# Optimization experiments

Hardware: AMD Instinct MI355X
Metric: run time of the kernel (lower is better)

The kernel has to match this reference:

```python
import jax, jax.numpy as jnp
import numpy as np

B, C, D = 65536, 64, 32

def setup_inputs() -> dict:
    key = jax.random.key(0)
    k1, k2 = jax.random.split(key)
    x = jax.random.normal(k1, (B, C, D), dtype=jnp.float32)
    W = jax.random.normal(k2, (C, D, D), dtype=jnp.float32)  # stacked per-channel Linear weights (torch inits to eye, but trainable)
    return {"x": x, "W": W}

def reference(x, W):
    # x: [B, C, D]; W: [C, D, D] with W[j] the weight of the j-th Linear(D,D,bias=False)
    Dd = W.shape[-1]
    b = x.shape[0]
    xr = x.reshape(b, -1, Dd)           # [B, C, D]
    xT = jnp.swapaxes(xr, 1, 2)          # [B, D, C] (k=D axis, channel last)
    # Ox[b,k,j] = sum_m W[j,k,m] * xT[b,m,j]  (per-channel tiny GEMM, batched)
    Ox = jnp.einsum('jkm,bmj->bkj', W, xT)
    # xOx[b,i] = sum_k sum_j xT[b,k,i] * Ox[b,k,j]
    xOx = jnp.einsum('bki,bkj->bi', xT, Ox)  # [B, C]
    return jnp.tanh(xOx)
```

## Files before the change

kernel.cpp:

```cpp
#include <hip/hip_runtime.h>
#include <cstdint>

typedef __attribute__((ext_vector_type(8))) short short8;
typedef __attribute__((ext_vector_type(4))) float f32x4;

__device__ __forceinline__ unsigned short bf16_rne(float f) {
    unsigned u = __float_as_uint(f);
    u += 0x7FFFu + ((u >> 16) & 1u);
    return (unsigned short)(u >> 16);
}

__global__ __launch_bounds__(1024) void wtab_kernel(const float* __restrict__ W,
                                                    unsigned short* __restrict__ tab) {
    int el = blockIdx.x * 1024 + threadIdx.x;
    int b    = el & 7;
    int lane = (el >> 3) & 63;
    int nh   = (el >> 9) & 1;
    int ks   = el >> 10;
    int e = ks * 32 + (lane >> 4) * 8 + b;
    int k = nh * 16 + (lane & 15);
    int jp = e >> 5, m = e & 31;
    float w = W[jp * 1024 + k * 32 + m];
    unsigned short hi = bf16_rne(w);
    float fh = __uint_as_float((unsigned)hi << 16);
    unsigned short lo = bf16_rne(w - fh);
    tab[(((ks * 2 + nh) * 2 + 0) * 64 + lane) * 8 + b] = hi;
    tab[(((ks * 2 + nh) * 2 + 1) * 64 + lane) * 8 + b] = lo;
}

__device__ __forceinline__ void split8(const float4& a, const float4& b,
                                       short8& hi, short8& lo) {
    float f[8] = {a.x, a.y, a.z, a.w, b.x, b.y, b.z, b.w};
    #pragma unroll
    for (int u = 0; u < 8; ++u) {
        unsigned short h = bf16_rne(f[u]);
        hi[u] = (short)h;
        float fh = __uint_as_float((unsigned)h << 16);
        lo[u] = (short)bf16_rne(f[u] - fh);
    }
}

__global__ __launch_bounds__(256) void ipf_kernel(const float* __restrict__ x,
                                                  const unsigned short* __restrict__ tab,
                                                  float* __restrict__ out) {
    __shared__ float Sl[4][16 * 36];
    const int t = threadIdx.x;
    const int w = t >> 6, l = t & 63;
    const long long b0 = ((long long)blockIdx.x * 4 + w) * 16;

    const float* xrow = x + (b0 + (l & 15)) * 2048 + (l >> 4) * 8;
    f32x4 c0 = {0.f, 0.f, 0.f, 0.f};
    f32x4 c1 = {0.f, 0.f, 0.f, 0.f};

    #pragma unroll 2
    for (int ks = 0; ks < 64; ++ks) {
        const float4 xa = *(const float4*)(xrow + ks * 32);
        const float4 xb = *(const float4*)(xrow + ks * 32 + 4);
        const short8* tp = (const short8*)(tab + ks * 2048);
        const short8 wh0 = tp[l];
        const short8 wl0 = tp[64 + l];
        const short8 wh1 = tp[128 + l];
        const short8 wl1 = tp[192 + l];
        short8 xhi, xlo;
        split8(xa, xb, xhi, xlo);
        c0 = __builtin_amdgcn_mfma_f32_16x16x32_bf16(xhi, wh0, c0, 0, 0, 0);
        c1 = __builtin_amdgcn_mfma_f32_16x16x32_bf16(xhi, wh1, c1, 0, 0, 0);
        c0 = __builtin_amdgcn_mfma_f32_16x16x32_bf16(xhi, wl0, c0, 0, 0, 0);
        c1 = __builtin_amdgcn_mfma_f32_16x16x32_bf16(xhi, wl1, c1, 0, 0, 0);
        c0 = __builtin_amdgcn_mfma_f32_16x16x32_bf16(xlo, wh0, c0, 0, 0, 0);
        c1 = __builtin_amdgcn_mfma_f32_16x16x32_bf16(xlo, wh1, c1, 0, 0, 0);
    }

    float* S = &Sl[w][0];
    #pragma unroll
    for (int r = 0; r < 4; ++r) {
        S[((l >> 4) * 4 + r) * 36 + (l & 15)]      = c0[r];
        S[((l >> 4) * 4 + r) * 36 + 16 + (l & 15)] = c1[r];
    }
    asm volatile("s_waitcnt lgkmcnt(0)" ::: "memory");

    const float* xb2 = x + b0 * 2048;
    #pragma unroll 1
    for (int r = 0; r < 16; ++r) {
        const float* xr = xb2 + r * 2048 + l * 32;
        const float* sr = S + r * 36;
        float s = 0.0f;
        #pragma unroll
        for (int q = 0; q < 8; ++q) {
            const float4 xv = *(const float4*)(xr + q * 4);
            s += xv.x * sr[q * 4] + xv.y * sr[q * 4 + 1]
               + xv.z * sr[q * 4 + 2] + xv.w * sr[q * 4 + 3];
        }
        const float e2 = __expf(2.0f * s);
        out[(b0 + r) * 64 + l] = 1.0f - 2.0f / (e2 + 1.0f);
    }
}

extern "C" void kernel_launch(void* const* d_in, const int* in_sizes, int n_in,
                              void* d_out, int out_size, void* d_ws, size_t ws_size,
                              hipStream_t stream) {
    const float* x = (const float*)d_in[0];
    const float* W = (const float*)d_in[1];
    float* out = (float*)d_out;
    unsigned short* tab = (unsigned short*)d_ws;

    wtab_kernel<<<64, 1024, 0, stream>>>(W, tab);
    ipf_kernel<<<1024, 256, 0, stream>>>(x, tab, out);
}
```

Before: 207.2 us.

## Stream x through LDS ring buffer with async global-to-LDS loads, reuse for second phase

Restructures the main kernel to process 256 batch rows per block, streaming x into an 18-slot LDS ring buffer via global_load_lds with swizzled addresses and a two-deep prefetch. The first-phase MFMA work is split across waves by k-half and ks-half, with partial sums folded through LDS. The second dot product then reads x back from LDS instead of global memory, lagging 16 slots behind. This removes the second global read of x and overlaps loads with compute, at the cost of many barriers per iteration, one block per CU, and a large LDS footprint.

```diff
diff --git a/kernel.cpp b/kernel.cpp
--- a/kernel.cpp
+++ b/kernel.cpp
@@ -3,6 +3,12 @@
 
 typedef __attribute__((ext_vector_type(8))) short short8;
 typedef __attribute__((ext_vector_type(4))) float f32x4;
+typedef const __attribute__((address_space(1))) uint32_t gu32;
+typedef __attribute__((address_space(3))) uint32_t lu32;
+
+#define NB    18
+#define CHB   8192
+#define NSLOT 256
 
 __device__ __forceinline__ unsigned short bf16_rne(float f) {
     unsigned u = __float_as_uint(f);
@@ -28,6 +34,12 @@
     tab[(((ks * 2 + nh) * 2 + 1) * 64 + lane) * 8 + b] = lo;
 }
 
+template <int CTRL>
+__device__ __forceinline__ float dpp_add(float v) {
+    int moved = __builtin_amdgcn_update_dpp(0, __float_as_int(v), CTRL, 0xF, 0xF, true);
+    return v + __int_as_float(moved);
+}
+
 __device__ __forceinline__ void split8(const float4& a, const float4& b,
                                        short8& hi, short8& lo) {
     float f[8] = {a.x, a.y, a.z, a.w, b.x, b.y, b.z, b.w};
@@ -40,60 +52,121 @@
     }
 }
 
-__global__ __launch_bounds__(256) void ipf_kernel(const float* __restrict__ x,
-                                                  const unsigned short* __restrict__ tab,
-                                                  float* __restrict__ out) {
-    __shared__ float Sl[4][16 * 36];
+__global__ __launch_bounds__(256, 1) void ipf_kernel(const float* __restrict__ x,
+                                                     const unsigned short* __restrict__ tab,
+                                                     float* __restrict__ out) {
+    extern __shared__ char smem[];
+    char* xbuf = smem;
+    float* Sp = (float*)(smem + NB * CHB);
+    float* Sl = Sp + 4 * 16 * 17;
     const int t = threadIdx.x;
     const int w = t >> 6, l = t & 63;
-    const long long b0 = ((long long)blockIdx.x * 4 + w) * 16;
+    const int kh = w & 1, eh = w >> 1;
+    const long long base = (long long)blockIdx.x * 256;
+    const char* gx = (const char*)(x + base * 2048);
 
-    const float* xrow = x + (b0 + (l & 15)) * 2048 + (l >> 4) * 8;
-    f32x4 c0 = {0.f, 0.f, 0.f, 0.f};
-    f32x4 c1 = {0.f, 0.f, 0.f, 0.f};
+    f32x4 c = {0.f, 0.f, 0.f, 0.f};
 
-    #pragma unroll 2
-    for (int ks = 0; ks < 64; ++ks) {
-        const float4 xa = *(const float4*)(xrow + ks * 32);
-        const float4 xb = *(const float4*)(xrow + ks * 32 + 4);
-        const short8* tp = (const short8*)(tab + ks * 2048);
-        const short8 wh0 = tp[l];
-        const short8 wl0 = tp[64 + l];
-        const short8 wh1 = tp[128 + l];
-        const short8 wl1 = tp[192 + l];
-        short8 xhi, xlo;
-        split8(xa, xb, xhi, xlo);
-        c0 = __builtin_amdgcn_mfma_f32_16x16x32_bf16(xhi, wh0, c0, 0, 0, 0);
-        c1 = __builtin_amdgcn_mfma_f32_16x16x32_bf16(xhi, wh1, c1, 0, 0, 0);
-        c0 = __builtin_amdgcn_mfma_f32_16x16x32_bf16(xhi, wl0, c0, 0, 0, 0);
-        c1 = __builtin_amdgcn_mfma_f32_16x16x32_bf16(xhi, wl1, c1, 0, 0, 0);
-        c0 = __builtin_amdgcn_mfma_f32_16x16x32_bf16(xlo, wh0, c0, 0, 0, 0);
-        c1 = __builtin_amdgcn_mfma_f32_16x16x32_bf16(xlo, wh1, c1, 0, 0, 0);
+    auto STAGE = [&](int n) {
+        const int bn = n % NB;
+        const size_t tb = (size_t)(n >> 4) * 131072 + (size_t)(n & 15) * 512;
+        #pragma unroll
+        for (int u = 0; u < 2; ++u) {
+            const int row = w * 4 + u * 2 + (l >> 5);
+            const char* gs = gx + tb + (size_t)row * 8192
+                           + (((l & 31) * 16) ^ ((row & 7) * 16));
+            __builtin_amdgcn_global_load_lds((gu32*)gs,
+                (lu32*)(xbuf + bn * CHB + w * 2048 + u * 1024), 16, 0, 0);
+        }
+    };
+
+    auto PH2 = [&](int m) {
+        const int bm = m % NB, cm = m & 15, tp = m >> 4, sb = tp & 1;
+        const int did = l >> 2, sub = l & 3;
+        const int b = w * 4 + (did >> 2), il = did & 3;
+        const int key = (b & 7) * 16;
+        const char* rp = xbuf + bm * CHB + b * 512;
+        const int fb = il * 128 + sub * 32;
+        const float4 x0 = *(const float4*)(rp + (fb ^ key));
+        const float4 x1 = *(const float4*)(rp + ((fb + 16) ^ key));
+        const float* sp = Sl + sb * 576 + b * 36 + sub * 8;
+        const float4 s0 = *(const float4*)sp;
+        const float4 s1 = *(const float4*)(sp + 4);
+        float s = x0.x * s0.x + x0.y * s0.y + x0.z * s0.z + x0.w * s0.w
+                + x1.x * s1.x + x1.y * s1.y + x1.z * s1.z + x1.w * s1.w;
+        s = dpp_add<0x111>(s);
+        s = dpp_add<0x112>(s);
+        if (sub == 3) {
+            const float e2 = __expf(2.0f * s);
+            out[(base + tp * 16 + b) * 64 + cm * 4 + il] = 1.0f - 2.0f / (e2 + 1.0f);
+        }
+    };
+
+    auto FOLD = [&](int tile) {
+        #pragma unroll
+        for (int rr = 0; rr < 4; ++rr)
+            Sp[w * 272 + ((l >> 4) * 4 + rr) * 17 + (l & 15)] = c[rr];
+        c[0] = 0.f; c[1] = 0.f; c[2] = 0.f; c[3] = 0.f;
+        asm volatile("s_waitcnt lgkmcnt(0)" ::: "memory");
+        __builtin_amdgcn_s_barrier();
+        const int sb = tile & 1;
+        #pragma unroll
+        for (int u = 0; u < 2; ++u) {
+            const int sidx = t + u * 256;
+            const int b_ = sidx >> 5, k_ = sidx & 31;
+            const int kh_ = k_ >> 4, kk_ = k_ & 15;
+            Sl[sb * 576 + b_ * 36 + k_] =
+                Sp[kh_ * 272 + b_ * 17 + kk_] + Sp[(kh_ + 2) * 272 + b_ * 17 + kk_];
+        }
+        asm volatile("s_waitcnt lgkmcnt(0)" ::: "memory");
+        __builtin_amdgcn_s_barrier();
+    };
+
+    STAGE(0);
+    STAGE(1);
+
+    #pragma unroll 1
+    for (int n = 0; n < NSLOT; ++n) {
+        if ((n & 15) == 0 && n > 0) FOLD((n >> 4) - 1);
+        if (n < NSLOT - 1) asm volatile("s_waitcnt vmcnt(2)" ::: "memory");
+        else               asm volatile("s_waitcnt vmcnt(0)" ::: "memory");
+        __builtin_amdgcn_s_barrier();
+        __builtin_amdgcn_sched_barrier(0);
+
+        {
+            const int bn = n % NB;
+            const int r = l & 15, h = l >> 4;
+            const int key = (r & 7) * 16;
+            const char* rp = xbuf + bn * CHB + r * 512;
+            #pragma unroll
+            for (int q2 = 0; q2 < 2; ++q2) {
+                const int ksl = 2 * eh + q2;
+                const int ksg = (n & 15) * 4 + ksl;
+                const int fb = ksl * 128 + h * 32;
+                const float4 xa  = *(const float4*)(rp + (fb ^ key));
+                const float4 xb2 = *(const float4*)(rp + ((fb + 16) ^ key));
+                const short8* tpp = (const short8*)(tab + (size_t)ksg * 2048 + kh * 1024) + l;
+                const short8 wh = tpp[0];
+                const short8 wl = tpp[64];
+                short8 xhi, xlo;
+                split8(xa, xb2, xhi, xlo);
+                c = __builtin_amdgcn_mfma_f32_16x16x32_bf16(xhi, wh, c, 0, 0, 0);
+                c = __builtin_amdgcn_mfma_f32_16x16x32_bf16(xhi, wl, c, 0, 0, 0);
+                c = __builtin_amdgcn_mfma_f32_16x16x32_bf16(xlo, wh, c, 0, 0, 0);
+            }
+        }
+
+        if (n >= 16) PH2(n - 16);
+
+        asm volatile("s_waitcnt lgkmcnt(0)" ::: "memory");
+        __builtin_amdgcn_s_barrier();
+        __builtin_amdgcn_sched_barrier(0);
+        if (n + 2 < NSLOT) STAGE(n + 2);
     }
 
-    float* S = &Sl[w][0];
-    #pragma unroll
-    for (int r = 0; r < 4; ++r) {
-        S[((l >> 4) * 4 + r) * 36 + (l & 15)]      = c0[r];
-        S[((l >> 4) * 4 + r) * 36 + 16 + (l & 15)] = c1[r];
-    }
-    asm volatile("s_waitcnt lgkmcnt(0)" ::: "memory");
-
-    const float* xb2 = x + b0 * 2048;
+    FOLD(15);
     #pragma unroll 1
-    for (int r = 0; r < 16; ++r) {
-        const float* xr = xb2 + r * 2048 + l * 32;
-        const float* sr = S + r * 36;
-        float s = 0.0f;
-        #pragma unroll
-        for (int q = 0; q < 8; ++q) {
-            const float4 xv = *(const float4*)(xr + q * 4);
-            s += xv.x * sr[q * 4] + xv.y * sr[q * 4 + 1]
-               + xv.z * sr[q * 4 + 2] + xv.w * sr[q * 4 + 3];
-        }
-        const float e2 = __expf(2.0f * s);
-        out[(b0 + r) * 64 + l] = 1.0f - 2.0f / (e2 + 1.0f);
-    }
+    for (int m = NSLOT - 16; m < NSLOT; ++m) PH2(m);
 }
 
 extern "C" void kernel_launch(void* const* d_in, const int* in_sizes, int n_in,
@@ -104,6 +177,10 @@
     float* out = (float*)d_out;
     unsigned short* tab = (unsigned short*)d_ws;
 
+    const size_t smem_bytes = (size_t)NB * CHB + (4 * 16 * 17 + 2 * 16 * 36) * sizeof(float);
+    hipFuncSetAttribute((const void*)ipf_kernel,
+                        hipFuncAttributeMaxDynamicSharedMemorySize, (int)smem_bytes);
+
     wtab_kernel<<<64, 1024, 0, stream>>>(W, tab);
-    ipf_kernel<<<1024, 256, 0, stream>>>(x, tab, out);
+    ipf_kernel<<<256, 256, smem_bytes, stream>>>(x, tab, out);
 }
```

New measurement: 308.1 us. +48.7%, slower.

## Stream x through per-wave LDS ring with async global_load_lds prefetch

Applied to the files above, without the earlier changes.

Replaces direct global loads of x in both phases with asynchronous global-to-LDS copies into a per-wave ring buffer (4-deep for the MFMA phase, 2-deep for the reduction phase), using XOR swizzling to avoid bank conflicts. Explicit vmcnt waits and sched barriers keep loads two stages ahead of compute. The aim is to hide memory latency and get coalesced, wide loads. In exchange LDS use rises to about 75 KB per block, which may lower occupancy, and the hand-tuned vmcnt counts are fragile.

```diff
diff --git a/kernel.cpp b/kernel.cpp
--- a/kernel.cpp
+++ b/kernel.cpp
@@ -3,6 +3,10 @@
 
 typedef __attribute__((ext_vector_type(8))) short short8;
 typedef __attribute__((ext_vector_type(4))) float f32x4;
+typedef const __attribute__((address_space(1))) uint32_t gu32;
+typedef __attribute__((address_space(3))) uint32_t lu32;
+
+#define WLDS 18688
 
 __device__ __forceinline__ unsigned short bf16_rne(float f) {
     unsigned u = __float_as_uint(f);
@@ -43,56 +47,105 @@
 __global__ __launch_bounds__(256) void ipf_kernel(const float* __restrict__ x,
                                                   const unsigned short* __restrict__ tab,
                                                   float* __restrict__ out) {
-    __shared__ float Sl[4][16 * 36];
+    extern __shared__ char smem[];
     const int t = threadIdx.x;
     const int w = t >> 6, l = t & 63;
+    char* ring = smem + w * WLDS;
+    float* Sl = (float*)(ring + 16384);
     const long long b0 = ((long long)blockIdx.x * 4 + w) * 16;
+    const char* gxt = (const char*)(x + b0 * 2048);
 
-    const float* xrow = x + (b0 + (l & 15)) * 2048 + (l >> 4) * 8;
+    auto STAGE1 = [&](int c) {
+        char* ld = ring + (c & 3) * 4096;
+        #pragma unroll
+        for (int u = 0; u < 4; ++u) {
+            const int row = u * 4 + (l >> 4);
+            const char* gs = gxt + (size_t)row * 8192 + c * 256
+                           + (((l & 15) * 16) ^ ((row & 7) * 16));
+            __builtin_amdgcn_global_load_lds((gu32*)gs, (lu32*)(ld + u * 1024), 16, 0, 0);
+        }
+    };
+    auto STAGE2 = [&](int r) {
+        const char* gs = gxt + (size_t)r * 8192;
+        char* ld = ring + (r & 1) * 8192;
+        #pragma unroll
+        for (int u = 0; u < 8; ++u)
+            __builtin_amdgcn_global_load_lds((gu32*)(gs + u * 1024 + l * 16),
+                                             (lu32*)(ld + u * 1024), 16, 0, 0);
+    };
+
     f32x4 c0 = {0.f, 0.f, 0.f, 0.f};
     f32x4 c1 = {0.f, 0.f, 0.f, 0.f};
 
-    #pragma unroll 2
-    for (int ks = 0; ks < 64; ++ks) {
-        const float4 xa = *(const float4*)(xrow + ks * 32);
-        const float4 xb = *(const float4*)(xrow + ks * 32 + 4);
-        const short8* tp = (const short8*)(tab + ks * 2048);
-        const short8 wh0 = tp[l];
-        const short8 wl0 = tp[64 + l];
-        const short8 wh1 = tp[128 + l];
-        const short8 wl1 = tp[192 + l];
-        short8 xhi, xlo;
-        split8(xa, xb, xhi, xlo);
-        c0 = __builtin_amdgcn_mfma_f32_16x16x32_bf16(xhi, wh0, c0, 0, 0, 0);
-        c1 = __builtin_amdgcn_mfma_f32_16x16x32_bf16(xhi, wh1, c1, 0, 0, 0);
-        c0 = __builtin_amdgcn_mfma_f32_16x16x32_bf16(xhi, wl0, c0, 0, 0, 0);
-        c1 = __builtin_amdgcn_mfma_f32_16x16x32_bf16(xhi, wl1, c1, 0, 0, 0);
-        c0 = __builtin_amdgcn_mfma_f32_16x16x32_bf16(xlo, wh0, c0, 0, 0, 0);
-        c1 = __builtin_amdgcn_mfma_f32_16x16x32_bf16(xlo, wh1, c1, 0, 0, 0);
+    STAGE1(0);
+    STAGE1(1);
+
+    const int row = l & 15;
+    const int key = (row & 7) * 16;
+    #pragma unroll 1
+    for (int c = 0; c < 32; ++c) {
+        if (c == 0)      asm volatile("s_waitcnt vmcnt(4)" ::: "memory");
+        else if (c < 31) asm volatile("s_waitcnt vmcnt(12)" ::: "memory");
+        else             asm volatile("s_waitcnt vmcnt(8)" ::: "memory");
+        __builtin_amdgcn_sched_barrier(0);
+
+        const char* cb = ring + (c & 3) * 4096 + row * 256;
+        #pragma unroll
+        for (int ksl = 0; ksl < 2; ++ksl) {
+            const int p = (l >> 4) * 2 + ksl * 8;
+            const float4 xa  = *(const float4*)(cb + ((p * 16) ^ key));
+            const float4 xb2 = *(const float4*)(cb + (((p + 1) * 16) ^ key));
+            const int ksg = c * 2 + ksl;
+            const short8* tp = (const short8*)(tab + (size_t)ksg * 2048);
+            const short8 wh0 = tp[l];
+            const short8 wl0 = tp[64 + l];
+            const short8 wh1 = tp[128 + l];
+            const short8 wl1 = tp[192 + l];
+            short8 xhi, xlo;
+            split8(xa, xb2, xhi, xlo);
+            c0 = __builtin_amdgcn_mfma_f32_16x16x32_bf16(xhi, wh0, c0, 0, 0, 0);
+            c1 = __builtin_amdgcn_mfma_f32_16x16x32_bf16(xhi, wh1, c1, 0, 0, 0);
+            c0 = __builtin_amdgcn_mfma_f32_16x16x32_bf16(xhi, wl0, c0, 0, 0, 0);
+            c1 = __builtin_amdgcn_mfma_f32_16x16x32_bf16(xhi, wl1, c1, 0, 0, 0);
+            c0 = __builtin_amdgcn_mfma_f32_16x16x32_bf16(xlo, wh0, c0, 0, 0, 0);
+            c1 = __builtin_amdgcn_mfma_f32_16x16x32_bf16(xlo, wh1, c1, 0, 0, 0);
+        }
+        __builtin_amdgcn_sched_barrier(0);
+        if (c + 2 < 32) STAGE1(c + 2);
     }
 
-    float* S = &Sl[w][0];
     #pragma unroll
-    for (int r = 0; r < 4; ++r) {
-        S[((l >> 4) * 4 + r) * 36 + (l & 15)]      = c0[r];
-        S[((l >> 4) * 4 + r) * 36 + 16 + (l & 15)] = c1[r];
+    for (int rr = 0; rr < 4; ++rr) {
+        Sl[((l >> 4) * 4 + rr) * 36 + (l & 15)]      = c0[rr];
+        Sl[((l >> 4) * 4 + rr) * 36 + 16 + (l & 15)] = c1[rr];
     }
     asm volatile("s_waitcnt lgkmcnt(0)" ::: "memory");
+    __builtin_amdgcn_sched_barrier(0);
 
-    const float* xb2 = x + b0 * 2048;
+    STAGE2(0);
+    STAGE2(1);
+
     #pragma unroll 1
     for (int r = 0; r < 16; ++r) {
-        const float* xr = xb2 + r * 2048 + l * 32;
-        const float* sr = S + r * 36;
+        if (r == 0)      asm volatile("s_waitcnt vmcnt(8)" ::: "memory");
+        else if (r < 15) asm volatile("s_waitcnt vmcnt(9)" ::: "memory");
+        else             asm volatile("s_waitcnt vmcnt(1)" ::: "memory");
+        __builtin_amdgcn_sched_barrier(0);
+
+        const char* rb = ring + (r & 1) * 8192;
+        const float* sp = Sl + r * 36;
         float s = 0.0f;
         #pragma unroll
         for (int q = 0; q < 8; ++q) {
-            const float4 xv = *(const float4*)(xr + q * 4);
-            s += xv.x * sr[q * 4] + xv.y * sr[q * 4 + 1]
-               + xv.z * sr[q * 4 + 2] + xv.w * sr[q * 4 + 3];
+            const int p = (q + l) & 7;
+            const float4 xv = *(const float4*)(rb + l * 128 + p * 16);
+            const float4 sv = *(const float4*)(sp + p * 4);
+            s += xv.x * sv.x + xv.y * sv.y + xv.z * sv.z + xv.w * sv.w;
         }
         const float e2 = __expf(2.0f * s);
         out[(b0 + r) * 64 + l] = 1.0f - 2.0f / (e2 + 1.0f);
+        __builtin_amdgcn_sched_barrier(0);
+        if (r + 2 < 16) STAGE2(r + 2);
     }
 }
 
@@ -104,6 +157,10 @@
     float* out = (float*)d_out;
     unsigned short* tab = (unsigned short*)d_ws;
 
+    const size_t smem_bytes = 4 * WLDS;
+    hipFuncSetAttribute((const void*)ipf_kernel,
+                        hipFuncAttributeMaxDynamicSharedMemorySize, (int)smem_bytes);
+
     wtab_kernel<<<64, 1024, 0, stream>>>(W, tab);
-    ipf_kernel<<<1024, 256, 0, stream>>>(x, tab, out);
+    ipf_kernel<<<1024, 256, smem_bytes, stream>>>(x, tab, out);
 }
```

After: 200.6 us. 3.1% less time.
